# Kernel tuning notes

Hardware: AMD Instinct MI355X
Metric: run time of the kernel (lower is better)

The kernel has to match this reference:

```python
import jax, jax.numpy as jnp
import numpy as np

NUM_HEADS = 8
KEY_DIM = 32
ATTN_RATIO = 4
RESOLUTION = 7
VAL_DIM = KEY_DIM * ATTN_RATIO  # 128
SCALE = KEY_DIM ** (-0.5)


def _bias_idxs():
    # (2, N) grid positions, N = resolution^2
    r = RESOLUTION
    gh, gw = np.meshgrid(np.arange(r), np.arange(r), indexing='ij')
    pos = np.stack([gh, gw], 0).reshape(2, -1)
    rel = np.abs(pos[:, :, None] - pos[:, None, :])
    return jnp.asarray(rel[0] * r + rel[1], dtype=jnp.int32)  # (N, N)


def setup_inputs() -> dict:
    key = jax.random.key(0)
    ks = jax.random.split(key, 4)
    B, N, D = 2048, RESOLUTION * RESOLUTION, 384
    qkv_out = KEY_DIM * NUM_HEADS * 2 + VAL_DIM * NUM_HEADS  # 1536
    return {
        'x': jax.random.normal(ks[0], (B, N, D), jnp.float32),
        'qkv_kernel': jax.random.normal(ks[1], (D, qkv_out), jnp.float32) * 0.02,
        'qkv_bias': jnp.zeros((qkv_out,), jnp.float32),
        'proj_kernel': jax.random.normal(ks[2], (VAL_DIM * NUM_HEADS, D), jnp.float32) * 0.02,
        'proj_bias': jnp.zeros((D,), jnp.float32),
        'attention_biases': jax.random.normal(ks[3], (NUM_HEADS, N), jnp.float32) * 0.02,
    }


def reference(x, qkv_kernel, qkv_bias, proj_kernel, proj_bias, attention_biases):
    B, N, _ = x.shape
    idxs = _bias_idxs()  # (N, N) int32
    qkv = jnp.matmul(x, qkv_kernel) + qkv_bias            # (B, N, 1536)
    qkv = qkv.reshape(B, N, NUM_HEADS, -1).transpose(0, 2, 1, 3)  # (B, H, N, 2k+v)
    q = qkv[..., :KEY_DIM]
    k = qkv[..., KEY_DIM:2 * KEY_DIM]
    v = qkv[..., 2 * KEY_DIM:]
    attn = jnp.einsum('bhnd,bhmd->bhnm', q, k) * SCALE    # (B, H, N, N)
    bias = attention_biases[:, idxs]                       # (H, N, N) gather
    attn = jax.nn.softmax(attn + bias, axis=-1)
    out = jnp.einsum('bhnm,bhmd->bhnd', attn, v)           # (B, H, N, val_dim)
    out = out.transpose(0, 2, 1, 3).reshape(B, N, NUM_HEADS * VAL_DIM)
    return jnp.matmul(out, proj_kernel) + proj_bias
```

## Files before the change

### kernel.cpp

```cpp
#include <hip/hip_runtime.h>
#include <hip/hip_bf16.h>

using bf16x8 = short __attribute__((ext_vector_type(8)));
using f32x16 = float __attribute__((ext_vector_type(16)));

#define MROWS 100352
#define SCALE_Q 0.17677669529663687f

static __device__ __forceinline__ unsigned short f2bs(float f){
  unsigned u = __builtin_bit_cast(unsigned, f);
  unsigned r = (u + 0x7FFFu + ((u >> 16) & 1u)) >> 16;
  return (unsigned short)r;
}
static __device__ __forceinline__ unsigned packbf(float a, float b){
  return (unsigned)f2bs(a) | ((unsigned)f2bs(b) << 16);
}

__global__ void k_xcast(const float* __restrict__ x, short* __restrict__ xb){
  const int i = blockIdx.x*256 + threadIdx.x;
  const float4 u0 = *reinterpret_cast<const float4*>(x + (size_t)i*8);
  const float4 u1 = *reinterpret_cast<const float4*>(x + (size_t)i*8 + 4);
  bf16x8 t;
  t[0]=(short)f2bs(u0.x); t[1]=(short)f2bs(u0.y); t[2]=(short)f2bs(u0.z); t[3]=(short)f2bs(u0.w);
  t[4]=(short)f2bs(u1.x); t[5]=(short)f2bs(u1.y); t[6]=(short)f2bs(u1.z); t[7]=(short)f2bs(u1.w);
  *reinterpret_cast<bf16x8*>(xb + (size_t)i*8) = t;
}

__global__ void k_convert(const float* __restrict__ qkvW, const float* __restrict__ qkvB,
                          const float* __restrict__ projW, const float* __restrict__ ab,
                          short* __restrict__ WqkvT, short* __restrict__ WpT,
                          float* __restrict__ bqkv, float* __restrict__ bias_exp){
  int i = blockIdx.x*256 + threadIdx.x;
  if (i < 1536*384){
    int c = i/384, f = i - c*384;
    int src; float sc = 1.0f;
    if (c < 512){ src = (c>>6)*192 + (c&63); if ((c&63) < 32) sc = SCALE_Q; }
    else        { int dv = c - 512; src = (dv>>7)*192 + 64 + (dv&127); }
    WqkvT[i] = (short)f2bs(qkvW[f*1536 + src] * sc);
    return;
  }
  i -= 1536*384;
  if (i < 384*1024){
    int j = i/1024, m = i - j*1024;
    WpT[i] = (short)f2bs(projW[m*384 + j]);
    return;
  }
  i -= 384*1024;
  if (i < 1536){
    int c = i; int src; float sc = 1.0f;
    if (c < 512){ src = (c>>6)*192 + (c&63); if ((c&63) < 32) sc = SCALE_Q; }
    else        { int dv = c - 512; src = (dv>>7)*192 + 64 + (dv&127); }
    bqkv[c] = qkvB[src] * sc;
    return;
  }
  i -= 1536;
  if (i < 8*64*49){
    int h = i / (64*49), rem = i - h*(64*49);
    int r = rem / 49, n = rem - r*49;
    float v = 0.0f;
    if (r < 49){
      int rh = r/7, rw = r - rh*7, ch = n/7, cw = n - ch*7;
      int dh = rh>ch?rh-ch:ch-rh, dw = rw>cw?rw-cw:cw-rw;
      v = ab[h*49 + dh*7 + dw];
    }
    bias_exp[i] = v;
  }
}

template<int KTOT, bool F32OUT>
__global__ __launch_bounds__(256) void k_gemm(const short* __restrict__ A,
                                              const short* __restrict__ Bw,
                                              const float* __restrict__ bias,
                                              void* __restrict__ Cout, int ldc){
  __shared__ short Alds[128*64];
  __shared__ short Blds[128*64];
  const int lane = threadIdx.x & 63, w = threadIdx.x >> 6;
  const int hi = lane >> 5, l31 = lane & 31;
  const int wm = w >> 1, wn = w & 1;
  const size_t R0 = (size_t)blockIdx.x*128, C0 = (size_t)blockIdx.y*128;

  f32x16 acc[2][2];
  acc[0][0]=(f32x16)0.f; acc[0][1]=(f32x16)0.f; acc[1][0]=(f32x16)0.f; acc[1][1]=(f32x16)0.f;

  const int srow = lane >> 3;
  const int sG   = ((lane & 7) ^ srow) * 8;
  const short* aG = A  + (R0 + (size_t)(w*8 + srow))*KTOT + sG;
  const short* bG = Bw + (C0 + (size_t)(w*8 + srow))*KTOT + sG;

  constexpr int NK = KTOT/64;
  for (int kt=0; kt<NK; ++kt){
    #pragma unroll
    for (int j=0; j<4; ++j){
      __builtin_amdgcn_global_load_lds(
        (const unsigned int __attribute__((address_space(1)))*)(aG + (size_t)j*32*KTOT + kt*64),
        (unsigned int __attribute__((address_space(3)))*)(&Alds[(j*32 + w*8)*64]), 16, 0, 0);
      __builtin_amdgcn_global_load_lds(
        (const unsigned int __attribute__((address_space(1)))*)(bG + (size_t)j*32*KTOT + kt*64),
        (unsigned int __attribute__((address_space(3)))*)(&Blds[(j*32 + w*8)*64]), 16, 0, 0);
    }
    __syncthreads();
    #pragma unroll
    for (int ks=0; ks<4; ++ks){
      bf16x8 aF[2], bF[2];
      #pragma unroll
      for (int mt=0; mt<2; ++mt){
        const int rA = wm*64 + mt*32 + l31;
        aF[mt] = *reinterpret_cast<const bf16x8*>(
                   (const char*)Alds + rA*128 + ((((ks<<1)|hi) ^ (rA&7))<<4));
      }
      #pragma unroll
      for (int nt=0; nt<2; ++nt){
        const int rB = wn*64 + nt*32 + l31;
        bF[nt] = *reinterpret_cast<const bf16x8*>(
                   (const char*)Blds + rB*128 + ((((ks<<1)|hi) ^ (rB&7))<<4));
      }
      #pragma unroll
      for (int mt=0; mt<2; ++mt)
        #pragma unroll
        for (int nt=0; nt<2; ++nt)
          acc[mt][nt] = __builtin_amdgcn_mfma_f32_32x32x16_bf16(aF[mt], bF[nt], acc[mt][nt], 0,0,0);
    }
    __syncthreads();
  }

  #pragma unroll
  for (int nt=0; nt<2; ++nt){
    const int c = (int)C0 + wn*64 + nt*32 + l31;
    const float bb = bias[c];
    #pragma unroll
    for (int mt=0; mt<2; ++mt){
      const size_t rbase = R0 + wm*64 + mt*32;
      #pragma unroll
      for (int rg=0; rg<16; ++rg){
        const size_t r = rbase + (rg&3) + 8*(rg>>2) + 4*hi;
        if constexpr (F32OUT) ((float*)Cout)[r*ldc + c] = acc[mt][nt][rg] + bb;
        else                  ((short*)Cout)[r*ldc + c] = (short)f2bs(acc[mt][nt][rg] + bb);
      }
    }
  }
}

__global__ __launch_bounds__(256) void k_attn(const short* __restrict__ qkvbuf,
                                              const float* __restrict__ bias_exp, short* __restrict__ aout){
  const int lane = threadIdx.x & 63, w = threadIdx.x >> 6;
  const int hi = lane >> 5, l31 = lane & 31;
  const int b = blockIdx.x, hg = blockIdx.y;
  const int h = hg*4 + w;

  __shared__ short vlds[4*49*136];

  for (int i=0; i<13; ++i){
    const int n = i*4 + w;
    if (n < 49){
      const bf16x8 vv = *reinterpret_cast<const bf16x8*>(qkvbuf + (b*49+n)*1536 + 512 + hg*512 + lane*8);
      const int hh = lane >> 4;
      const int d0 = ((lane & 15) * 8) ^ (((n>>3)&1) << 5);
      *reinterpret_cast<bf16x8*>(&vlds[(hh*49 + n)*136 + d0]) = vv;
    }
  }
  __syncthreads();

  bf16x8 kf[2][2];
  #pragma unroll
  for (int mt=0; mt<2; ++mt){
    const int n = 32*mt + l31;
    #pragma unroll
    for (int ks=0; ks<2; ++ks)
      kf[mt][ks] = (n < 49)
        ? *reinterpret_cast<const bf16x8*>(qkvbuf + (b*49+n)*1536 + h*64 + 32 + ks*16 + hi*8)
        : (bf16x8)(short)0;
  }
  const short* vb = &vlds[w*49*136];
  const int dxbase = hi << 5;

  for (int rb=0; rb<2; ++rb){
    const int r = 32*rb + l31;
    bf16x8 qf[2];
    #pragma unroll
    for (int ks=0; ks<2; ++ks)
      qf[ks] = (r < 49)
        ? *reinterpret_cast<const bf16x8*>(qkvbuf + (b*49+r)*1536 + h*64 + ks*16 + hi*8)
        : (bf16x8)(short)0;

    f32x16 s[2];
    s[0] = (f32x16)0.0f; s[1] = (f32x16)0.0f;
    #pragma unroll
    for (int ks=0; ks<2; ++ks){
      s[0] = __builtin_amdgcn_mfma_f32_32x32x16_bf16(kf[0][ks], qf[ks], s[0], 0, 0, 0);
      s[1] = __builtin_amdgcn_mfma_f32_32x32x16_bf16(kf[1][ks], qf[ks], s[1], 0, 0, 0);
    }

    float mloc = -3.0e38f;
    #pragma unroll
    for (int mt=0; mt<2; ++mt)
      #pragma unroll
      for (int rg=0; rg<16; ++rg){
        const int n = 32*mt + (rg&3) + 8*(rg>>2) + 4*hi;
        float v = s[mt][rg];
        v = (n < 49) ? v + bias_exp[(h*64 + r)*49 + n] : -1.0e30f;
        s[mt][rg] = v;
        mloc = fmaxf(mloc, v);
      }
    const float mrow = fmaxf(mloc, __shfl_xor(mloc, 32));
    float sloc = 0.0f;
    #pragma unroll
    for (int mt=0; mt<2; ++mt)
      #pragma unroll
      for (int rg=0; rg<16; ++rg){
        const float p = __expf(s[mt][rg] - mrow);
        s[mt][rg] = p; sloc += p;
      }
    const float inv = 1.0f / (sloc + __shfl_xor(sloc, 32));
    #pragma unroll
    for (int mt=0; mt<2; ++mt)
      #pragma unroll
      for (int rg=0; rg<16; ++rg) s[mt][rg] *= inv;

    unsigned pk[8][2];
    #pragma unroll
    for (int o=0; o<8; ++o){
      const int mt = o>>2, base = 4*(o&3);
      pk[o][0] = packbf(s[mt][base+0], s[mt][base+1]);
      pk[o][1] = packbf(s[mt][base+2], s[mt][base+3]);
    }
    bf16x8 af[4];
    #pragma unroll
    for (int ks=0; ks<4; ++ks){
      const unsigned e0 = pk[2*ks][0],   e1 = pk[2*ks][1];
      const unsigned o0 = pk[2*ks+1][0], o1 = pk[2*ks+1][1];
      const unsigned own0 = hi ? o0 : e0, own1 = hi ? o1 : e1;
      const unsigned oth0 = hi ? e0 : o0, oth1 = hi ? e1 : o1;
      const unsigned sw0 = __shfl_xor(oth0, 32), sw1 = __shfl_xor(oth1, 32);
      const unsigned lo0 = hi ? sw0 : own0, lo1 = hi ? sw1 : own1;
      const unsigned h0  = hi ? own0 : sw0, h1  = hi ? own1 : sw1;
      union { bf16x8 v; unsigned u[4]; } t;
      t.u[0]=lo0; t.u[1]=lo1; t.u[2]=h0; t.u[3]=h1;
      af[ks] = t.v;
    }

    #pragma unroll
    for (int dt=0; dt<4; ++dt){
      const int dx = (dt*32 + l31) ^ dxbase;
      f32x16 acc = (f32x16)0.0f;
      #pragma unroll
      for (int ks=0; ks<4; ++ks){
        bf16x8 t;
        if (ks < 3){
          const int nb = ks*16 + hi*8;
          #pragma unroll
          for (int j=0; j<8; ++j) t[j] = vb[(nb + j)*136 + dx];
        } else {
          #pragma unroll
          for (int j=0; j<8; ++j) t[j] = 0;
          if (hi == 0) t[0] = vb[48*136 + (dt*32 + l31)];
        }
        acc = __builtin_amdgcn_mfma_f32_32x32x16_bf16(af[ks], t, acc, 0, 0, 0);
      }
      #pragma unroll
      for (int rg=0; rg<16; ++rg){
        const int rr = 32*rb + (rg&3) + 8*(rg>>2) + 4*hi;
        if (rr < 49)
          aout[(b*49+rr)*1024 + h*128 + dt*32 + l31] = (short)f2bs(acc[rg]);
      }
    }
  }
}

extern "C" void kernel_launch(void* const* d_in, const int* in_sizes, int n_in,
                              void* d_out, int out_size, void* d_ws, size_t ws_size,
                              hipStream_t stream) {
  const float* x     = (const float*)d_in[0];
  const float* qkvW  = (const float*)d_in[1];
  const float* qkvB  = (const float*)d_in[2];
  const float* projW = (const float*)d_in[3];
  const float* projB = (const float*)d_in[4];
  const float* ab    = (const float*)d_in[5];

  char* ws = (char*)d_ws;
  short* aoutb = (short*)ws;
  short* xb    = (short*)ws;
  size_t off = (size_t)MROWS*1024*2;
  short* qkvbuf = (short*)(ws + off); off += (size_t)MROWS*1536*2;
  short* WqkvT  = (short*)(ws + off); off += (size_t)1536*384*2;
  short* WpT    = (short*)(ws + off); off += (size_t)384*1024*2;
  float* bqkv   = (float*)(ws + off); off += (size_t)1536*4;
  float* bias_exp = (float*)(ws + off); off += (size_t)8*64*49*4;
  if (ws_size < off) return;

  const int conv_total = 1536*384 + 384*1024 + 1536 + 8*64*49;
  k_convert<<<(conv_total + 255)/256, 256, 0, stream>>>(qkvW, qkvB, projW, ab,
                                                        WqkvT, WpT, bqkv, bias_exp);
  k_xcast<<<MROWS*384/8/256, 256, 0, stream>>>(x, xb);
  k_gemm<384,false><<<dim3(784, 12), 256, 0, stream>>>(xb, WqkvT, bqkv, qkvbuf, 1536);
  k_attn<<<dim3(2048, 2), 256, 0, stream>>>(qkvbuf, bias_exp, aoutb);
  k_gemm<1024,true><<<dim3(784, 3), 256, 0, stream>>>(aoutb, WpT, projB, d_out, 384);
}
```

Baseline: 526.7 us.

## Widen GEMM tiles to 512 threads with XCD-aware block swizzle

The GEMM kernel moves to 8 waves per block with a templated N tile (256 columns for the QKV GEMM, 384 for the projection). Each block now reuses one A panel across more output columns, so A is re-read from memory fewer times. Block indices are remapped with a swizzle over groups of 8, likely to keep blocks that share A panels on the same XCD/L2. The costs are more LDS and accumulator registers per block, which may lower occupancy; the projection GEMM drops to 784 blocks, which may leave CUs underfilled.

```diff
diff --git a/kernel.cpp b/kernel.cpp
--- a/kernel.cpp
+++ b/kernel.cpp
@@ -67,20 +67,29 @@
   }
 }
 
-template<int KTOT, bool F32OUT>
-__global__ __launch_bounds__(256) void k_gemm(const short* __restrict__ A,
+template<int KTOT, int NT, int NSLAB, bool F32OUT>
+__global__ __launch_bounds__(512) void k_gemm(const short* __restrict__ A,
                                               const short* __restrict__ Bw,
                                               const float* __restrict__ bias,
                                               void* __restrict__ Cout, int ldc){
+  constexpr int BN = NT*128;
   __shared__ short Alds[128*64];
-  __shared__ short Blds[128*64];
+  __shared__ short Blds[BN*64];
   const int lane = threadIdx.x & 63, w = threadIdx.x >> 6;
   const int hi = lane >> 5, l31 = lane & 31;
-  const int wm = w >> 1, wn = w & 1;
-  const size_t R0 = (size_t)blockIdx.x*128, C0 = (size_t)blockIdx.y*128;
-
-  f32x16 acc[2][2];
-  acc[0][0]=(f32x16)0.f; acc[0][1]=(f32x16)0.f; acc[1][0]=(f32x16)0.f; acc[1][1]=(f32x16)0.f;
+  const int wm = w >> 2, wn = w & 3;
+
+  const int nwg = NSLAB * 784;
+  const int lin = blockIdx.x + NSLAB * blockIdx.y;
+  const int swz = (lin & 7) * (nwg >> 3) + (lin >> 3);
+  const int slab = swz % NSLAB, panel = swz / NSLAB;
+  const size_t R0 = (size_t)panel * 128, C0 = (size_t)slab * BN;
+
+  f32x16 acc[2][NT];
+  #pragma unroll
+  for (int mt=0; mt<2; ++mt)
+    #pragma unroll
+    for (int nt=0; nt<NT; ++nt) acc[mt][nt] = (f32x16)0.0f;
 
   const int srow = lane >> 3;
   const int sG   = ((lane & 7) ^ srow) * 8;
@@ -90,18 +99,19 @@
   constexpr int NK = KTOT/64;
   for (int kt=0; kt<NK; ++kt){
     #pragma unroll
-    for (int j=0; j<4; ++j){
+    for (int j=0; j<2; ++j)
       __builtin_amdgcn_global_load_lds(
-        (const unsigned int __attribute__((address_space(1)))*)(aG + (size_t)j*32*KTOT + kt*64),
-        (unsigned int __attribute__((address_space(3)))*)(&Alds[(j*32 + w*8)*64]), 16, 0, 0);
+        (const unsigned int __attribute__((address_space(1)))*)(aG + (size_t)j*64*KTOT + kt*64),
+        (unsigned int __attribute__((address_space(3)))*)(&Alds[(j*64 + w*8)*64]), 16, 0, 0);
+    #pragma unroll
+    for (int j=0; j<2*NT; ++j)
       __builtin_amdgcn_global_load_lds(
-        (const unsigned int __attribute__((address_space(1)))*)(bG + (size_t)j*32*KTOT + kt*64),
-        (unsigned int __attribute__((address_space(3)))*)(&Blds[(j*32 + w*8)*64]), 16, 0, 0);
-    }
+        (const unsigned int __attribute__((address_space(1)))*)(bG + (size_t)j*64*KTOT + kt*64),
+        (unsigned int __attribute__((address_space(3)))*)(&Blds[(j*64 + w*8)*64]), 16, 0, 0);
     __syncthreads();
     #pragma unroll
     for (int ks=0; ks<4; ++ks){
-      bf16x8 aF[2], bF[2];
+      bf16x8 aF[2], bF[NT];
       #pragma unroll
       for (int mt=0; mt<2; ++mt){
         const int rA = wm*64 + mt*32 + l31;
@@ -109,23 +119,23 @@
                    (const char*)Alds + rA*128 + ((((ks<<1)|hi) ^ (rA&7))<<4));
       }
       #pragma unroll
-      for (int nt=0; nt<2; ++nt){
-        const int rB = wn*64 + nt*32 + l31;
+      for (int nt=0; nt<NT; ++nt){
+        const int rB = wn*(NT*32) + nt*32 + l31;
         bF[nt] = *reinterpret_cast<const bf16x8*>(
                    (const char*)Blds + rB*128 + ((((ks<<1)|hi) ^ (rB&7))<<4));
       }
       #pragma unroll
       for (int mt=0; mt<2; ++mt)
         #pragma unroll
-        for (int nt=0; nt<2; ++nt)
+        for (int nt=0; nt<NT; ++nt)
           acc[mt][nt] = __builtin_amdgcn_mfma_f32_32x32x16_bf16(aF[mt], bF[nt], acc[mt][nt], 0,0,0);
     }
     __syncthreads();
   }
 
   #pragma unroll
-  for (int nt=0; nt<2; ++nt){
-    const int c = (int)C0 + wn*64 + nt*32 + l31;
+  for (int nt=0; nt<NT; ++nt){
+    const int c = (int)C0 + wn*(NT*32) + nt*32 + l31;
     const float bb = bias[c];
     #pragma unroll
     for (int mt=0; mt<2; ++mt){
@@ -291,7 +301,7 @@
   k_convert<<<(conv_total + 255)/256, 256, 0, stream>>>(qkvW, qkvB, projW, ab,
                                                         WqkvT, WpT, bqkv, bias_exp);
   k_xcast<<<MROWS*384/8/256, 256, 0, stream>>>(x, xb);
-  k_gemm<384,false><<<dim3(784, 12), 256, 0, stream>>>(xb, WqkvT, bqkv, qkvbuf, 1536);
+  k_gemm<384, 2, 6, false><<<dim3(6, 784), 512, 0, stream>>>(xb, WqkvT, bqkv, qkvbuf, 1536);
   k_attn<<<dim3(2048, 2), 256, 0, stream>>>(qkvbuf, bias_exp, aoutb);
-  k_gemm<1024,true><<<dim3(784, 3), 256, 0, stream>>>(aoutb, WpT, projB, d_out, 384);
-}
+  k_gemm<1024, 3, 1, true><<<dim3(1, 784), 512, 0, stream>>>(aoutb, WpT, projB, d_out, 384);
+}
```

Measured after the change: 547.5 us. +4.0%, slower.

## Double-buffer GEMM LDS tiles, enlarge QKV tile, and swizzle workgroup order

Applied to the files above, without the earlier changes.

Replaces the generic single-buffered GEMM with two specialized kernels that double-buffer 32-wide K slices in LDS, so global-to-LDS loads for step k+2 are issued while step k computes, with explicit vmcnt waits and barriers. The QKV GEMM moves to 256x256 tiles with 512 threads for more reuse per tile, and both kernels remap block indices with an XCD-style swizzle so neighbouring panels share cache. The goal is to hide global-load latency and cut redundant operand traffic. The cost is more LDS and registers per block, which may lower occupancy.

```diff
diff --git a/kernel.cpp b/kernel.cpp
--- a/kernel.cpp
+++ b/kernel.cpp
@@ -67,74 +67,194 @@
   }
 }
 
-template<int KTOT, bool F32OUT>
-__global__ __launch_bounds__(256) void k_gemm(const short* __restrict__ A,
-                                              const short* __restrict__ Bw,
-                                              const float* __restrict__ bias,
-                                              void* __restrict__ Cout, int ldc){
-  __shared__ short Alds[128*64];
-  __shared__ short Blds[128*64];
-  const int lane = threadIdx.x & 63, w = threadIdx.x >> 6;
+__global__ __launch_bounds__(512) void k_qkv6(const short* __restrict__ xb,
+                                              const short* __restrict__ WqkvT,
+                                              const float* __restrict__ bqkv,
+                                              short* __restrict__ qkvbuf){
+  __shared__ short Alds[2][256*32];
+  __shared__ short Blds[2][256*32];
+  const int t = threadIdx.x;
+  const int lane = t & 63, w = t >> 6;
   const int hi = lane >> 5, l31 = lane & 31;
   const int wm = w >> 1, wn = w & 1;
-  const size_t R0 = (size_t)blockIdx.x*128, C0 = (size_t)blockIdx.y*128;
+
+  const int nwg = 6*392;
+  const int lin = blockIdx.x + 6*blockIdx.y;
+  const int swz = (lin & 7)*(nwg>>3) + (lin>>3);
+  const int slab = swz % 6, panel = swz / 6;
+  const size_t R0 = (size_t)panel*256, C0 = (size_t)slab*256;
+
+  const int srowl  = lane >> 2;
+  const int schunk = ((lane & 3) ^ ((lane >> 3) & 3)) * 8;
+  const short* aG0 = xb    + (R0 + (size_t)(w*16       + srowl))*384 + schunk;
+  const short* aG1 = xb    + (R0 + (size_t)((8+w)*16   + srowl))*384 + schunk;
+  const short* bG0 = WqkvT + (C0 + (size_t)(w*16       + srowl))*384 + schunk;
+  const short* bG1 = WqkvT + (C0 + (size_t)((8+w)*16   + srowl))*384 + schunk;
+
+  auto stage = [&](int bufi, int kti){
+    __builtin_amdgcn_global_load_lds((const unsigned __attribute__((address_space(1)))*)(aG0 + kti*32),
+        (unsigned __attribute__((address_space(3)))*)(&Alds[bufi][w*512]), 16, 0, 0);
+    __builtin_amdgcn_global_load_lds((const unsigned __attribute__((address_space(1)))*)(aG1 + kti*32),
+        (unsigned __attribute__((address_space(3)))*)(&Alds[bufi][(8+w)*512]), 16, 0, 0);
+    __builtin_amdgcn_global_load_lds((const unsigned __attribute__((address_space(1)))*)(bG0 + kti*32),
+        (unsigned __attribute__((address_space(3)))*)(&Blds[bufi][w*512]), 16, 0, 0);
+    __builtin_amdgcn_global_load_lds((const unsigned __attribute__((address_space(1)))*)(bG1 + kti*32),
+        (unsigned __attribute__((address_space(3)))*)(&Blds[bufi][(8+w)*512]), 16, 0, 0);
+  };
+
+  f32x16 acc[2][4];
+  #pragma unroll
+  for (int mt=0; mt<2; ++mt)
+    #pragma unroll
+    for (int nt=0; nt<4; ++nt) acc[mt][nt] = (f32x16)0.0f;
+
+  stage(0, 0); stage(1, 1);
+
+  #define QKV_COMPUTE(CUR)                                                              \
+    _Pragma("unroll")                                                                   \
+    for (int ks=0; ks<2; ++ks){                                                         \
+      bf16x8 aF[2], bF[4];                                                              \
+      _Pragma("unroll")                                                                 \
+      for (int mt=0; mt<2; ++mt){                                                       \
+        const int rA = wm*64 + mt*32 + l31;                                             \
+        aF[mt] = *reinterpret_cast<const bf16x8*>(                                      \
+          (const char*)&Alds[CUR][0] + rA*64 + ((((ks<<1)|hi) ^ ((rA>>1)&3))<<4));      \
+      }                                                                                 \
+      _Pragma("unroll")                                                                 \
+      for (int nt=0; nt<4; ++nt){                                                       \
+        const int rB = wn*128 + nt*32 + l31;                                            \
+        bF[nt] = *reinterpret_cast<const bf16x8*>(                                      \
+          (const char*)&Blds[CUR][0] + rB*64 + ((((ks<<1)|hi) ^ ((rB>>1)&3))<<4));      \
+      }                                                                                 \
+      _Pragma("unroll")                                                                 \
+      for (int mt=0; mt<2; ++mt)                                                        \
+        _Pragma("unroll")                                                               \
+        for (int nt=0; nt<4; ++nt)                                                      \
+          acc[mt][nt] = __builtin_amdgcn_mfma_f32_32x32x16_bf16(aF[mt], bF[nt], acc[mt][nt], 0,0,0); \
+    }
+
+  for (int kt=0; kt<11; ++kt){
+    const int cur = kt & 1;
+    asm volatile("s_waitcnt vmcnt(4)" ::: "memory");
+    __builtin_amdgcn_sched_barrier(0);
+    __builtin_amdgcn_s_barrier();
+    QKV_COMPUTE(cur)
+    __builtin_amdgcn_s_barrier();
+    __builtin_amdgcn_sched_barrier(0);
+    if (kt < 10) stage(cur, kt+2);
+  }
+  asm volatile("s_waitcnt vmcnt(0)" ::: "memory");
+  __builtin_amdgcn_sched_barrier(0);
+  __builtin_amdgcn_s_barrier();
+  QKV_COMPUTE(1)
+  #undef QKV_COMPUTE
+
+  #pragma unroll
+  for (int nt=0; nt<4; ++nt){
+    const int c = (int)C0 + wn*128 + nt*32 + l31;
+    const float bb = bqkv[c];
+    #pragma unroll
+    for (int mt=0; mt<2; ++mt){
+      const size_t rbase = R0 + wm*64 + mt*32;
+      #pragma unroll
+      for (int rg=0; rg<16; ++rg){
+        const size_t r = rbase + (rg&3) + 8*(rg>>2) + 4*hi;
+        qkvbuf[r*1536 + c] = (short)f2bs(acc[mt][nt][rg] + bb);
+      }
+    }
+  }
+}
+
+__global__ __launch_bounds__(256) void k_proj6(const short* __restrict__ A,
+                                               const short* __restrict__ WpT,
+                                               const float* __restrict__ pb,
+                                               float* __restrict__ out){
+  __shared__ short Alds[2][128*32];
+  __shared__ short Blds[2][128*32];
+  const int t = threadIdx.x;
+  const int lane = t & 63, w = t >> 6;
+  const int hi = lane >> 5, l31 = lane & 31;
+  const int wm = w >> 1, wn = w & 1;
+
+  const int nwg = 3*784;
+  const int lin = blockIdx.x + 3*blockIdx.y;
+  const int swz = (lin & 7)*(nwg>>3) + (lin>>3);
+  const int slab = swz % 3, panel = swz / 3;
+  const size_t R0 = (size_t)panel*128, C0 = (size_t)slab*128;
+
+  const int srowl  = lane >> 2;
+  const int schunk = ((lane & 3) ^ ((lane >> 3) & 3)) * 8;
+  const short* aG0 = A   + (R0 + (size_t)(w*16     + srowl))*1024 + schunk;
+  const short* aG1 = A   + (R0 + (size_t)((4+w)*16 + srowl))*1024 + schunk;
+  const short* bG0 = WpT + (C0 + (size_t)(w*16     + srowl))*1024 + schunk;
+  const short* bG1 = WpT + (C0 + (size_t)((4+w)*16 + srowl))*1024 + schunk;
+
+  auto stage = [&](int bufi, int kti){
+    __builtin_amdgcn_global_load_lds((const unsigned __attribute__((address_space(1)))*)(aG0 + kti*32),
+        (unsigned __attribute__((address_space(3)))*)(&Alds[bufi][w*512]), 16, 0, 0);
+    __builtin_amdgcn_global_load_lds((const unsigned __attribute__((address_space(1)))*)(aG1 + kti*32),
+        (unsigned __attribute__((address_space(3)))*)(&Alds[bufi][(4+w)*512]), 16, 0, 0);
+    __builtin_amdgcn_global_load_lds((const unsigned __attribute__((address_space(1)))*)(bG0 + kti*32),
+        (unsigned __attribute__((address_space(3)))*)(&Blds[bufi][w*512]), 16, 0, 0);
+    __builtin_amdgcn_global_load_lds((const unsigned __attribute__((address_space(1)))*)(bG1 + kti*32),
+        (unsigned __attribute__((address_space(3)))*)(&Blds[bufi][(4+w)*512]), 16, 0, 0);
+  };
 
   f32x16 acc[2][2];
   acc[0][0]=(f32x16)0.f; acc[0][1]=(f32x16)0.f; acc[1][0]=(f32x16)0.f; acc[1][1]=(f32x16)0.f;
 
-  const int srow = lane >> 3;
-  const int sG   = ((lane & 7) ^ srow) * 8;
-  const short* aG = A  + (R0 + (size_t)(w*8 + srow))*KTOT + sG;
-  const short* bG = Bw + (C0 + (size_t)(w*8 + srow))*KTOT + sG;
-
-  constexpr int NK = KTOT/64;
-  for (int kt=0; kt<NK; ++kt){
-    #pragma unroll
-    for (int j=0; j<4; ++j){
-      __builtin_amdgcn_global_load_lds(
-        (const unsigned int __attribute__((address_space(1)))*)(aG + (size_t)j*32*KTOT + kt*64),
-        (unsigned int __attribute__((address_space(3)))*)(&Alds[(j*32 + w*8)*64]), 16, 0, 0);
-      __builtin_amdgcn_global_load_lds(
-        (const unsigned int __attribute__((address_space(1)))*)(bG + (size_t)j*32*KTOT + kt*64),
-        (unsigned int __attribute__((address_space(3)))*)(&Blds[(j*32 + w*8)*64]), 16, 0, 0);
-    }
-    __syncthreads();
-    #pragma unroll
-    for (int ks=0; ks<4; ++ks){
-      bf16x8 aF[2], bF[2];
-      #pragma unroll
-      for (int mt=0; mt<2; ++mt){
-        const int rA = wm*64 + mt*32 + l31;
-        aF[mt] = *reinterpret_cast<const bf16x8*>(
-                   (const char*)Alds + rA*128 + ((((ks<<1)|hi) ^ (rA&7))<<4));
-      }
-      #pragma unroll
-      for (int nt=0; nt<2; ++nt){
-        const int rB = wn*64 + nt*32 + l31;
-        bF[nt] = *reinterpret_cast<const bf16x8*>(
-                   (const char*)Blds + rB*128 + ((((ks<<1)|hi) ^ (rB&7))<<4));
-      }
-      #pragma unroll
-      for (int mt=0; mt<2; ++mt)
-        #pragma unroll
-        for (int nt=0; nt<2; ++nt)
-          acc[mt][nt] = __builtin_amdgcn_mfma_f32_32x32x16_bf16(aF[mt], bF[nt], acc[mt][nt], 0,0,0);
-    }
-    __syncthreads();
-  }
+  stage(0, 0); stage(1, 1);
+
+  #define PROJ_COMPUTE(CUR)                                                             \
+    _Pragma("unroll")                                                                   \
+    for (int ks=0; ks<2; ++ks){                                                         \
+      bf16x8 aF[2], bF[2];                                                              \
+      _Pragma("unroll")                                                                 \
+      for (int mt=0; mt<2; ++mt){                                                       \
+        const int rA = wm*64 + mt*32 + l31;                                             \
+        aF[mt] = *reinterpret_cast<const bf16x8*>(                                      \
+          (const char*)&Alds[CUR][0] + rA*64 + ((((ks<<1)|hi) ^ ((rA>>1)&3))<<4));      \
+      }                                                                                 \
+      _Pragma("unroll")                                                                 \
+      for (int nt=0; nt<2; ++nt){                                                       \
+        const int rB = wn*64 + nt*32 + l31;                                             \
+        bF[nt] = *reinterpret_cast<const bf16x8*>(                                      \
+          (const char*)&Blds[CUR][0] + rB*64 + ((((ks<<1)|hi) ^ ((rB>>1)&3))<<4));      \
+      }                                                                                 \
+      _Pragma("unroll")                                                                 \
+      for (int mt=0; mt<2; ++mt)                                                        \
+        _Pragma("unroll")                                                               \
+        for (int nt=0; nt<2; ++nt)                                                      \
+          acc[mt][nt] = __builtin_amdgcn_mfma_f32_32x32x16_bf16(aF[mt], bF[nt], acc[mt][nt], 0,0,0); \
+    }
+
+  for (int kt=0; kt<31; ++kt){
+    const int cur = kt & 1;
+    asm volatile("s_waitcnt vmcnt(4)" ::: "memory");
+    __builtin_amdgcn_sched_barrier(0);
+    __builtin_amdgcn_s_barrier();
+    PROJ_COMPUTE(cur)
+    __builtin_amdgcn_s_barrier();
+    __builtin_amdgcn_sched_barrier(0);
+    if (kt < 30) stage(cur, kt+2);
+  }
+  asm volatile("s_waitcnt vmcnt(0)" ::: "memory");
+  __builtin_amdgcn_sched_barrier(0);
+  __builtin_amdgcn_s_barrier();
+  PROJ_COMPUTE(1)
+  #undef PROJ_COMPUTE
 
   #pragma unroll
   for (int nt=0; nt<2; ++nt){
     const int c = (int)C0 + wn*64 + nt*32 + l31;
-    const float bb = bias[c];
+    const float bb = pb[c];
     #pragma unroll
     for (int mt=0; mt<2; ++mt){
       const size_t rbase = R0 + wm*64 + mt*32;
       #pragma unroll
       for (int rg=0; rg<16; ++rg){
         const size_t r = rbase + (rg&3) + 8*(rg>>2) + 4*hi;
-        if constexpr (F32OUT) ((float*)Cout)[r*ldc + c] = acc[mt][nt][rg] + bb;
-        else                  ((short*)Cout)[r*ldc + c] = (short)f2bs(acc[mt][nt][rg] + bb);
+        out[r*384 + c] = acc[mt][nt][rg] + bb;
       }
     }
   }
@@ -291,7 +411,7 @@
   k_convert<<<(conv_total + 255)/256, 256, 0, stream>>>(qkvW, qkvB, projW, ab,
                                                         WqkvT, WpT, bqkv, bias_exp);
   k_xcast<<<MROWS*384/8/256, 256, 0, stream>>>(x, xb);
-  k_gemm<384,false><<<dim3(784, 12), 256, 0, stream>>>(xb, WqkvT, bqkv, qkvbuf, 1536);
+  k_qkv6<<<dim3(6, 392), 512, 0, stream>>>(xb, WqkvT, bqkv, qkvbuf);
   k_attn<<<dim3(2048, 2), 256, 0, stream>>>(qkvbuf, bias_exp, aoutb);
-  k_gemm<1024,true><<<dim3(784, 3), 256, 0, stream>>>(aoutb, WpT, projB, d_out, 384);
-}
+  k_proj6<<<dim3(3, 784), 256, 0, stream>>>(aoutb, WpT, projB, (float*)d_out);
+}
```

After: 512.8 us. 2.6% less time.
